# Kernel optimization log

Measured on AMD Instinct MI355X. Metric: run time of the kernel, lower is better.

Reference implementation:

```python
import jax, jax.numpy as jnp
import numpy as np

B, T, C = 2, 2048, 1024
H, DK, OUT = 16, 64, 1024


def setup_inputs() -> dict:
    key = jax.random.key(0)
    k1, k2, k3, k4, k5 = jax.random.split(key, 5)
    glorot_qkv = (2.0 / (C + H * DK)) ** 0.5  # glorot_normal stddev for [C,H,DK]
    glorot_o = (2.0 / (H * DK + OUT)) ** 0.5
    return {
        "x": jax.random.normal(k1, (B, T, C), dtype=jnp.float32),
        "query_mat": jax.random.normal(k2, (C, H, DK), dtype=jnp.float32) * glorot_qkv,
        "key_mat": jax.random.normal(k3, (C, H, DK), dtype=jnp.float32) * glorot_qkv,
        "value_mat": jax.random.normal(k4, (C, H, DK), dtype=jnp.float32) * glorot_qkv,
        "linear_m1": jax.random.normal(k5, (H * DK, OUT), dtype=jnp.float32) * glorot_o,
    }


def reference(x, query_mat, key_mat, value_mat, linear_m1):
    # x: [B,T,C]; projections: [C,H,DK]
    q = jnp.einsum('btc,chd->bhtd', x, query_mat)
    k = jnp.einsum('btc,chd->bhtd', x, key_mat)
    v = jnp.einsum('btc,chd->bhtd', x, value_mat)
    d_k = query_mat.shape[-1]
    # NOTE: faithful to source, which MULTIPLIES by sqrt(d_k)
    w = jnp.einsum('bhtd,bhzd->bhtz', q, k) * (d_k ** 0.5)
    t = w.shape[-1]
    causal = jnp.tril(jnp.ones((t, t), dtype=bool))  # [T,T]
    w = jnp.where(causal, w, -jnp.inf)
    w = jax.nn.softmax(w, axis=-1)
    # dropout inactive (training=False)
    o = jnp.einsum('bhtz,bhzd->bhtd', w, v)
    o = o.transpose(0, 2, 1, 3).reshape(o.shape[0], o.shape[2], -1)  # [B,T,H*DK]
    return jnp.einsum('btc,cz->btz', o, linear_m1)
```

## Files before the change

kernel.cpp:

```cpp
#include <hip/hip_runtime.h>


typedef unsigned short u16;
typedef unsigned int u32;
typedef unsigned long long u64;
typedef __attribute__((ext_vector_type(8))) short bf16x8;
typedef __attribute__((ext_vector_type(4))) float f32x4;

__device__ inline u16 f2bf(float f) {
  union { float f; unsigned u; } v; v.f = f;
  unsigned r = v.u + 0x7FFFu + ((v.u >> 16) & 1u);
  return (u16)(r >> 16);
}
__device__ inline float bf2f(u16 h) {
  union { unsigned u; float f; } v; v.u = ((unsigned)h) << 16;
  return v.f;
}
__device__ inline void glds16(const u16* g, u16* s) {
  __builtin_amdgcn_global_load_lds(
      (const __attribute__((address_space(1))) u32*)g,
      (__attribute__((address_space(3))) u32*)s, 16, 0, 0);
}
#define MFMA __builtin_amdgcn_mfma_f32_16x16x32_bf16

__global__ __launch_bounds__(256) void prep(
    const float* __restrict__ x,
    const float* __restrict__ wq, const float* __restrict__ wk,
    const float* __restrict__ wv, const float* __restrict__ wo,
    u16* __restrict__ Xh, u16* __restrict__ Xl,
    u16* __restrict__ Wqh, u16* __restrict__ Wql,
    u16* __restrict__ Wkh, u16* __restrict__ Wkl,
    u16* __restrict__ Wvt, u16* __restrict__ Wot) {
  const int z = blockIdx.z;
  const int tid = threadIdx.x;
  if (z == 0) {
    const int bid = blockIdx.y * 32 + blockIdx.x;
#pragma unroll
    for (int k = 0; k < 4; k++) {
      int i = bid * 4096 + k * 1024 + tid * 4;
      float4 v = *(const float4*)(x + i);
      ushort4 h, l;
      h.x = f2bf(v.x); l.x = f2bf(v.x - bf2f(h.x));
      h.y = f2bf(v.y); l.y = f2bf(v.y - bf2f(h.y));
      h.z = f2bf(v.z); l.z = f2bf(v.z - bf2f(h.z));
      h.w = f2bf(v.w); l.w = f2bf(v.w - bf2f(h.w));
      *(ushort4*)(Xh + i) = h;
      *(ushort4*)(Xl + i) = l;
    }
    return;
  }
  __shared__ float tile[32][33];
  const float* W = (z == 1) ? wq : (z == 2) ? wk : (z == 3) ? wv : wo;
  const int bx = blockIdx.x * 32, by = blockIdx.y * 32;
  const int tx = tid & 31, ty = tid >> 5;
#pragma unroll
  for (int j = 0; j < 32; j += 8)
    tile[ty + j][tx] = W[(size_t)(by + ty + j) * 1024 + bx + tx];
  __syncthreads();
  if (z <= 2) {
    u16* Th = (z == 1) ? Wqh : Wkh;
    u16* Tl = (z == 1) ? Wql : Wkl;
#pragma unroll
    for (int j = 0; j < 32; j += 8) {
      float v = tile[tx][ty + j];
      u16 h = f2bf(v);
      size_t idx = (size_t)(bx + ty + j) * 1024 + by + tx;
      Th[idx] = h;
      Tl[idx] = f2bf(v - bf2f(h));
    }
  } else {
    u16* T = (z == 3) ? Wvt : Wot;
#pragma unroll
    for (int j = 0; j < 32; j += 8)
      T[(size_t)(bx + ty + j) * 1024 + by + tx] = f2bf(tile[tx][ty + j]);
  }
}

__global__ __launch_bounds__(256) void gemm_qkv(
    const u16* __restrict__ Xh, const u16* __restrict__ Xl,
    const u16* __restrict__ Wqh, const u16* __restrict__ Wql,
    const u16* __restrict__ Wkh, const u16* __restrict__ Wkl,
    const u16* __restrict__ Wvt,
    u16* __restrict__ Qh, u16* __restrict__ Ql,
    u16* __restrict__ Kh, u16* __restrict__ Kl,
    u16* __restrict__ Vt) {
  __shared__ u16 S[4][128][32];
  const int K = 1024;
  const int z = blockIdx.z;
  const bool split = (z < 2);
  const u16* Bh = (z == 0) ? Wqh : (z == 1) ? Wkh : Wvt;
  const u16* Bl = (z == 0) ? Wql : Wkl;
  const int tid = threadIdx.x;
  const int lane = tid & 63, wv = tid >> 6;
  const int quad = lane >> 4, lc = lane & 15;
  const int m0 = blockIdx.y * 128, n0 = blockIdx.x * 128;
  const int wm = (wv >> 1) * 64, wn = (wv & 1) * 64;
  const int lrow = lane >> 2, lk = (lane & 3) * 8;
  const u16* a0p = Xh + (size_t)(m0 + wv * 32 + lrow) * K + lk;
  const u16* a1p = a0p + 16 * K;
  const u16* al0p = Xl + (size_t)(m0 + wv * 32 + lrow) * K + lk;
  const u16* al1p = al0p + 16 * K;
  const u16* b0p = Bh + (size_t)(n0 + wv * 32 + lrow) * K + lk;
  const u16* b1p = b0p + 16 * K;
  const u16* bl0p = split ? (Bl + (size_t)(n0 + wv * 32 + lrow) * K + lk) : b0p;
  const u16* bl1p = bl0p + 16 * K;
  u16* sA0 = &S[0][wv * 32][0];      u16* sA1 = &S[0][wv * 32 + 16][0];
  u16* sAl0 = &S[1][wv * 32][0];     u16* sAl1 = &S[1][wv * 32 + 16][0];
  u16* sB0 = &S[2][wv * 32][0];      u16* sB1 = &S[2][wv * 32 + 16][0];
  u16* sBl0 = &S[3][wv * 32][0];     u16* sBl1 = &S[3][wv * 32 + 16][0];
  f32x4 acc[4][4];
#pragma unroll
  for (int i = 0; i < 4; i++)
#pragma unroll
    for (int j = 0; j < 4; j++) acc[i][j] = (f32x4){0.f, 0.f, 0.f, 0.f};
  for (int kc = 0; kc < K; kc += 32) {
    __syncthreads();
    glds16(a0p + kc, sA0); glds16(a1p + kc, sA1);
    glds16(b0p + kc, sB0); glds16(b1p + kc, sB1);
    if (split) {
      glds16(al0p + kc, sAl0); glds16(al1p + kc, sAl1);
      glds16(bl0p + kc, sBl0); glds16(bl1p + kc, sBl1);
    }
    __syncthreads();
    bf16x8 ah[4], al[4];
#pragma unroll
    for (int mt = 0; mt < 4; mt++)
      ah[mt] = *(const bf16x8*)&S[0][wm + mt * 16 + lc][quad * 8];
    if (split) {
#pragma unroll
      for (int mt = 0; mt < 4; mt++)
        al[mt] = *(const bf16x8*)&S[1][wm + mt * 16 + lc][quad * 8];
    }
#pragma unroll
    for (int nt = 0; nt < 4; nt++) {
      bf16x8 bfh = *(const bf16x8*)&S[2][wn + nt * 16 + lc][quad * 8];
#pragma unroll
      for (int mt = 0; mt < 4; mt++)
        acc[mt][nt] = MFMA(ah[mt], bfh, acc[mt][nt], 0, 0, 0);
      if (split) {
        bf16x8 bfl = *(const bf16x8*)&S[3][wn + nt * 16 + lc][quad * 8];
#pragma unroll
        for (int mt = 0; mt < 4; mt++) {
          acc[mt][nt] = MFMA(ah[mt], bfl, acc[mt][nt], 0, 0, 0);
          acc[mt][nt] = MFMA(al[mt], bfh, acc[mt][nt], 0, 0, 0);
        }
      }
    }
  }
  const int rb = quad * 4;
  if (z == 2) {
#pragma unroll
    for (int mt = 0; mt < 4; mt++)
#pragma unroll
      for (int nt = 0; nt < 4; nt++)
#pragma unroll
        for (int r = 0; r < 4; r++) {
          int m = m0 + wm + mt * 16 + rb + r, n = n0 + wn + nt * 16 + lc;
          int b = m >> 11, t = m & 2047, h = n >> 6, d = n & 63;
          Vt[((size_t)(b * 16 + h) * 64 + d) * 2048 + t] = f2bf(acc[mt][nt][r]);
        }
  } else {
    u16* Ch = (z == 0) ? Qh : Kh;
    u16* Cl = (z == 0) ? Ql : Kl;
    const float scale = (z == 0) ? 8.0f : 1.0f;
#pragma unroll
    for (int mt = 0; mt < 4; mt++)
#pragma unroll
      for (int nt = 0; nt < 4; nt++)
#pragma unroll
        for (int r = 0; r < 4; r++) {
          int m = m0 + wm + mt * 16 + rb + r, n = n0 + wn + nt * 16 + lc;
          int b = m >> 11, t = m & 2047, h = n >> 6, d = n & 63;
          float v = acc[mt][nt][r] * scale;
          u16 hv = f2bf(v);
          size_t idx = ((size_t)(b * 16 + h) * 2048 + t) * 64 + d;
          Ch[idx] = hv;
          Cl[idx] = f2bf(v - bf2f(hv));
        }
  }
}

__global__ __launch_bounds__(256) void gemm_out(const u16* __restrict__ A,
                                                const u16* __restrict__ Bt,
                                                float* __restrict__ C) {
  __shared__ u16 Sa[64][32], Sb[128][32];
  const int K = 1024, N = 1024;
  const int tid = threadIdx.x;
  const int lane = tid & 63, wv = tid >> 6;
  const int quad = lane >> 4, lc = lane & 15;
  const int m0 = blockIdx.y * 64, n0 = blockIdx.x * 128;
  const int wm = (wv >> 1) * 32, wn = (wv & 1) * 64;
  const int lrow = lane >> 2, lk = (lane & 3) * 8;
  const u16* ap = A + (size_t)(m0 + wv * 16 + lrow) * K + lk;
  const u16* b0p = Bt + (size_t)(n0 + wv * 32 + lrow) * K + lk;
  const u16* b1p = b0p + 16 * K;
  u16* sA = &Sa[wv * 16][0];
  u16* sB0 = &Sb[wv * 32][0];
  u16* sB1 = &Sb[wv * 32 + 16][0];
  f32x4 acc[2][4];
#pragma unroll
  for (int i = 0; i < 2; i++)
#pragma unroll
    for (int j = 0; j < 4; j++) acc[i][j] = (f32x4){0.f, 0.f, 0.f, 0.f};
  for (int kc = 0; kc < K; kc += 32) {
    __syncthreads();
    glds16(ap + kc, sA);
    glds16(b0p + kc, sB0);
    glds16(b1p + kc, sB1);
    __syncthreads();
    bf16x8 ah[2];
#pragma unroll
    for (int mt = 0; mt < 2; mt++)
      ah[mt] = *(const bf16x8*)&Sa[wm + mt * 16 + lc][quad * 8];
#pragma unroll
    for (int nt = 0; nt < 4; nt++) {
      bf16x8 bfh = *(const bf16x8*)&Sb[wn + nt * 16 + lc][quad * 8];
#pragma unroll
      for (int mt = 0; mt < 2; mt++)
        acc[mt][nt] = MFMA(ah[mt], bfh, acc[mt][nt], 0, 0, 0);
    }
  }
#pragma unroll
  for (int mt = 0; mt < 2; mt++)
#pragma unroll
    for (int nt = 0; nt < 4; nt++)
#pragma unroll
      for (int r = 0; r < 4; r++)
        C[(size_t)(m0 + wm + mt * 16 + quad * 4 + r) * N + n0 + wn + nt * 16 + lc] =
            acc[mt][nt][r];
}

__global__ __launch_bounds__(256, 2) void attn(const u16* __restrict__ Qh,
                                               const u16* __restrict__ Ql,
                                               const u16* __restrict__ Kh,
                                               const u16* __restrict__ Kl,
                                               const u16* __restrict__ Vt,
                                               u16* __restrict__ O16) {
  __shared__ u16 Khs[2][64][64], Kls[2][64][64], Vs[2][64][64];
  __shared__ u16 Ps[4][16][72];
  const int tid = threadIdx.x;
  const int lane = tid & 63, w = tid >> 6;
  const int quad = lane >> 4, lc = lane & 15;
  const int i = blockIdx.x;
  const int bh = i & 31;
  const int qb = 31 - (i >> 5);
  const int ng = qb + 1;
  const int tq = qb * 64 + w * 16 + lc;
  const size_t kbase = (size_t)bh * 2048 * 64;
  const size_t vbase = (size_t)bh * 64 * 2048;
  const size_t qoff = kbase + (size_t)tq * 64 + quad * 8;
  bf16x8 qh0 = *(const bf16x8*)(Qh + qoff);
  bf16x8 qh1 = *(const bf16x8*)(Qh + qoff + 32);
  bf16x8 ql0 = *(const bf16x8*)(Ql + qoff);
  bf16x8 ql1 = *(const bf16x8*)(Ql + qoff + 32);
  const int srow = lane >> 3;
  const int scol = (lane & 7) ^ srow;
  const u16* kg0 = Kh + kbase + (size_t)(w * 16 + srow) * 64 + scol * 8;
  const u16* lg0 = Kl + kbase + (size_t)(w * 16 + srow) * 64 + scol * 8;
  const u16* vg0 = Vt + vbase + (size_t)(w * 16 + srow) * 2048 + scol * 8;

  float mi = -3.0e38f, li = 0.f;
  f32x4 o[4];
#pragma unroll
  for (int d = 0; d < 4; d++) o[d] = (f32x4){0.f, 0.f, 0.f, 0.f};
  const int rx = lc & 7;

  {
    glds16(kg0, &Khs[0][w * 16][0]); glds16(kg0 + 8 * 64, &Khs[0][w * 16 + 8][0]);
    glds16(lg0, &Kls[0][w * 16][0]); glds16(lg0 + 8 * 64, &Kls[0][w * 16 + 8][0]);
    glds16(vg0, &Vs[0][w * 16][0]);  glds16(vg0 + 8 * 2048, &Vs[0][w * 16 + 8][0]);
  }
  for (int g = 0; g < ng; g++) {
    const int buf = g & 1;
    const int z0 = g * 64;
    __syncthreads();
    if (g + 1 < ng) {
      const int zn = (g + 1) * 64;
      const int nb = buf ^ 1;
      glds16(kg0 + (size_t)zn * 64, &Khs[nb][w * 16][0]);
      glds16(kg0 + (size_t)zn * 64 + 8 * 64, &Khs[nb][w * 16 + 8][0]);
      glds16(lg0 + (size_t)zn * 64, &Kls[nb][w * 16][0]);
      glds16(lg0 + (size_t)zn * 64 + 8 * 64, &Kls[nb][w * 16 + 8][0]);
      glds16(vg0 + zn, &Vs[nb][w * 16][0]);
      glds16(vg0 + zn + 8 * 2048, &Vs[nb][w * 16 + 8][0]);
    }
    f32x4 s[4];
#pragma unroll
    for (int tt = 0; tt < 4; tt++) {
      const int R = tt * 16 + lc;
      bf16x8 kh0 = *(const bf16x8*)&Khs[buf][R][(quad ^ rx) * 8];
      bf16x8 kh1 = *(const bf16x8*)&Khs[buf][R][((4 + quad) ^ rx) * 8];
      bf16x8 kl0 = *(const bf16x8*)&Kls[buf][R][(quad ^ rx) * 8];
      bf16x8 kl1 = *(const bf16x8*)&Kls[buf][R][((4 + quad) ^ rx) * 8];
      f32x4 sv = (f32x4){0.f, 0.f, 0.f, 0.f};
      sv = MFMA(kh0, qh0, sv, 0, 0, 0);
      sv = MFMA(kh1, qh1, sv, 0, 0, 0);
      sv = MFMA(kh0, ql0, sv, 0, 0, 0);
      sv = MFMA(kh1, ql1, sv, 0, 0, 0);
      sv = MFMA(kl0, qh0, sv, 0, 0, 0);
      sv = MFMA(kl1, qh1, sv, 0, 0, 0);
      s[tt] = sv;
    }
    if (g == ng - 1) {
#pragma unroll
      for (int tt = 0; tt < 4; tt++)
#pragma unroll
        for (int r = 0; r < 4; r++)
          if (z0 + tt * 16 + quad * 4 + r > tq) s[tt][r] = -3.0e38f;
    }
    float smax = -3.0e38f;
#pragma unroll
    for (int tt = 0; tt < 4; tt++)
#pragma unroll
      for (int r = 0; r < 4; r++) smax = fmaxf(smax, s[tt][r]);
    smax = fmaxf(smax, __shfl_xor(smax, 16));
    smax = fmaxf(smax, __shfl_xor(smax, 32));
    float mnew = fmaxf(mi, smax);
    float alpha = __expf(mi - mnew);
    mi = mnew;
    float rs = 0.f;
#pragma unroll
    for (int tt = 0; tt < 4; tt++) {
      union { u16 h[4]; u64 d; } pk;
#pragma unroll
      for (int r = 0; r < 4; r++) {
        float p = __expf(s[tt][r] - mnew);
        rs += p;
        pk.h[r] = f2bf(p);
      }
      *(u64*)&Ps[w][lc][tt * 16 + quad * 4] = pk.d;
    }
    li = li * alpha + rs;
#pragma unroll
    for (int d = 0; d < 4; d++) o[d] *= alpha;
    bf16x8 pf0 = *(const bf16x8*)&Ps[w][lc][quad * 8];
    bf16x8 pf1 = *(const bf16x8*)&Ps[w][lc][32 + quad * 8];
#pragma unroll
    for (int dd = 0; dd < 4; dd++) {
      const int R = dd * 16 + lc;
      bf16x8 va0 = *(const bf16x8*)&Vs[buf][R][(quad ^ rx) * 8];
      bf16x8 va1 = *(const bf16x8*)&Vs[buf][R][((4 + quad) ^ rx) * 8];
      o[dd] = MFMA(va0, pf0, o[dd], 0, 0, 0);
      o[dd] = MFMA(va1, pf1, o[dd], 0, 0, 0);
    }
  }
  li += __shfl_xor(li, 16);
  li += __shfl_xor(li, 32);
  const float rli = 1.0f / li;
  const int b = bh >> 4, hh = bh & 15;
  const size_t obase = ((size_t)(b * 2048 + tq)) * 1024 + hh * 64 + quad * 4;
#pragma unroll
  for (int dd = 0; dd < 4; dd++) {
    ushort4 ov;
    ov.x = f2bf(o[dd][0] * rli);
    ov.y = f2bf(o[dd][1] * rli);
    ov.z = f2bf(o[dd][2] * rli);
    ov.w = f2bf(o[dd][3] * rli);
    *(ushort4*)&O16[obase + dd * 16] = ov;
  }
}

extern "C" void kernel_launch(void* const* d_in, const int* in_sizes, int n_in,
                              void* d_out, int out_size, void* d_ws, size_t ws_size,
                              hipStream_t stream) {
  const float* x  = (const float*)d_in[0];
  const float* wq = (const float*)d_in[1];
  const float* wk = (const float*)d_in[2];
  const float* wv = (const float*)d_in[3];
  const float* wo = (const float*)d_in[4];

  char* w = (char*)d_ws;
  const size_t MB = 1u << 20;
  u16* Xh  = (u16*)(w + 0 * MB);
  u16* Xl  = (u16*)(w + 8 * MB);
  u16* Wqh = (u16*)(w + 16 * MB);
  u16* Wql = (u16*)(w + 18 * MB);
  u16* Wkh = (u16*)(w + 20 * MB);
  u16* Wkl = (u16*)(w + 22 * MB);
  u16* Wvt = (u16*)(w + 24 * MB);
  u16* Wot = (u16*)(w + 26 * MB);
  u16* Qhb = (u16*)(w + 28 * MB);
  u16* Qlb = (u16*)(w + 36 * MB);
  u16* Khb = (u16*)(w + 44 * MB);
  u16* Klb = (u16*)(w + 52 * MB);
  u16* Vtb = (u16*)(w + 60 * MB);
  u16* O16 = (u16*)(w + 0 * MB);

  hipLaunchKernelGGL(prep, dim3(32, 32, 5), dim3(256), 0, stream,
                     x, wq, wk, wv, wo, Xh, Xl, Wqh, Wql, Wkh, Wkl, Wvt, Wot);

  hipLaunchKernelGGL(gemm_qkv, dim3(8, 32, 3), dim3(256), 0, stream,
                     Xh, Xl, Wqh, Wql, Wkh, Wkl, Wvt, Qhb, Qlb, Khb, Klb, Vtb);

  hipLaunchKernelGGL(attn, dim3(1024), dim3(256), 0, stream,
                     Qhb, Qlb, Khb, Klb, Vtb, O16);

  hipLaunchKernelGGL(gemm_out, dim3(8, 64), dim3(256), 0, stream, O16, Wot, (float*)d_out);
}
```

Before: 215.0 us.

## Replace QKV and output GEMMs with double-buffered 256x128 pipelined gemm kernel

Both projection GEMMs now run through one templated kernel with 512 threads, 256x128 tiles, K-chunks of 64 and double-buffered LDS filled by async global-to-LDS loads. An XOR swizzle avoids LDS bank conflicts, and explicit vmcnt waits plus barriers and s_setprio interleave loads with MFMA work. The split-precision hi/lo terms are handled as extra K tiles (48 tiles instead of 16), so the three-product sum is kept. This aims to hide global memory latency and raise MFMA utilisation. The hand-scheduled barrier and waitcnt sequence is fragile and could race if counts are wrong, and the larger LDS footprint limits occupancy.

```diff
diff --git a/kernel.cpp b/kernel.cpp
--- a/kernel.cpp
+++ b/kernel.cpp
@@ -76,78 +76,103 @@
   }
 }
 
-__global__ __launch_bounds__(256) void gemm_qkv(
-    const u16* __restrict__ Xh, const u16* __restrict__ Xl,
-    const u16* __restrict__ Wqh, const u16* __restrict__ Wql,
-    const u16* __restrict__ Wkh, const u16* __restrict__ Wkl,
-    const u16* __restrict__ Wvt,
+#define BAR() do { asm volatile("" ::: "memory"); __builtin_amdgcn_s_barrier(); asm volatile("" ::: "memory"); } while (0)
+#define WAITV(N) asm volatile("s_waitcnt vmcnt(" #N ")" ::: "memory")
+#define SP(P) __builtin_amdgcn_s_setprio(P)
+
+template <int MODE>
+__global__ __launch_bounds__(512, 2) void gemm3(
+    const u16* __restrict__ Ah_, const u16* __restrict__ Al_,
+    const u16* __restrict__ BQh, const u16* __restrict__ BQl,
+    const u16* __restrict__ BKh, const u16* __restrict__ BKl,
+    const u16* __restrict__ BVt,
     u16* __restrict__ Qh, u16* __restrict__ Ql,
     u16* __restrict__ Kh, u16* __restrict__ Kl,
-    u16* __restrict__ Vt) {
-  __shared__ u16 S[4][128][32];
-  const int K = 1024;
-  const int z = blockIdx.z;
-  const bool split = (z < 2);
-  const u16* Bh = (z == 0) ? Wqh : (z == 1) ? Wkh : Wvt;
-  const u16* Bl = (z == 0) ? Wql : Wkl;
+    u16* __restrict__ Vt, float* __restrict__ Cout) {
+  __shared__ __align__(16) u16 As[2][256][64];
+  __shared__ __align__(16) u16 Bs[2][128][64];
+  const int z = (MODE == 0) ? blockIdx.z : 3;
+  const u16* Bh_ = (MODE == 1) ? BQh : (z == 0) ? BQh : (z == 1) ? BKh : BVt;
+  const u16* Bl_ = (z == 0) ? BQl : (z == 1) ? BKl : Bh_;
+  const int NT = (MODE == 0 && z < 2) ? 48 : 16;
   const int tid = threadIdx.x;
-  const int lane = tid & 63, wv = tid >> 6;
-  const int quad = lane >> 4, lc = lane & 15;
-  const int m0 = blockIdx.y * 128, n0 = blockIdx.x * 128;
-  const int wm = (wv >> 1) * 64, wn = (wv & 1) * 64;
-  const int lrow = lane >> 2, lk = (lane & 3) * 8;
-  const u16* a0p = Xh + (size_t)(m0 + wv * 32 + lrow) * K + lk;
-  const u16* a1p = a0p + 16 * K;
-  const u16* al0p = Xl + (size_t)(m0 + wv * 32 + lrow) * K + lk;
-  const u16* al1p = al0p + 16 * K;
-  const u16* b0p = Bh + (size_t)(n0 + wv * 32 + lrow) * K + lk;
-  const u16* b1p = b0p + 16 * K;
-  const u16* bl0p = split ? (Bl + (size_t)(n0 + wv * 32 + lrow) * K + lk) : b0p;
-  const u16* bl1p = bl0p + 16 * K;
-  u16* sA0 = &S[0][wv * 32][0];      u16* sA1 = &S[0][wv * 32 + 16][0];
-  u16* sAl0 = &S[1][wv * 32][0];     u16* sAl1 = &S[1][wv * 32 + 16][0];
-  u16* sB0 = &S[2][wv * 32][0];      u16* sB1 = &S[2][wv * 32 + 16][0];
-  u16* sBl0 = &S[3][wv * 32][0];     u16* sBl1 = &S[3][wv * 32 + 16][0];
+  const int lane = tid & 63, wid = tid >> 6;
+  const int quad = lane >> 4, lc = lane & 15, l7 = lane & 7;
+  const int m0 = blockIdx.y * 256, n0 = blockIdx.x * 128;
+  const int wm = (wid >> 1) * 64, wn = (wid & 1) * 64;
+  const int srow = lane >> 3;
+  const int schunk = (lane & 7) ^ (srow & 7);
+  const int ar0 = (wid >> 1) * 64 + (wid & 1) * 16;
+  const int br0 = wid * 16;
+  const size_t aG = (size_t)(m0 + ar0 + srow) * 1024 + schunk * 8;
+  const size_t bG = (size_t)(n0 + br0 + srow) * 1024 + schunk * 8;
+
+#define AREG(T) (((T) < 32) ? Ah_ : Al_)
+#define BREG(T) ((((T) >> 4) == 1) ? Bl_ : Bh_)
+#define COL(T) ((size_t)((T) & 15) * 64)
+#define ST_A0(T, BUF) do { const u16* g_ = AREG(T) + aG + COL(T); \
+    glds16(g_, &As[BUF][ar0][0]); glds16(g_ + 8 * 1024, &As[BUF][ar0 + 8][0]); } while (0)
+#define ST_A1(T, BUF) do { const u16* g_ = AREG(T) + aG + COL(T) + 32 * 1024; \
+    glds16(g_, &As[BUF][ar0 + 32][0]); glds16(g_ + 8 * 1024, &As[BUF][ar0 + 40][0]); } while (0)
+#define ST_B(T, BUF) do { const u16* g_ = BREG(T) + bG + COL(T); \
+    glds16(g_, &Bs[BUF][br0][0]); glds16(g_ + 8 * 1024, &Bs[BUF][br0 + 8][0]); } while (0)
+#define LD_A(BUF, MH) do { _Pragma("unroll") for (int m2 = 0; m2 < 2; m2++) \
+    { _Pragma("unroll") for (int kk = 0; kk < 2; kk++) \
+      afr[m2][kk] = *(const bf16x8*)&As[BUF][wm + (MH) * 32 + m2 * 16 + lc][((kk * 4 + quad) ^ l7) * 8]; } } while (0)
+#define LD_B(BUF) do { _Pragma("unroll") for (int n = 0; n < 4; n++) \
+    { _Pragma("unroll") for (int kk = 0; kk < 2; kk++) \
+      bfr[n][kk] = *(const bf16x8*)&Bs[BUF][wn + n * 16 + lc][((kk * 4 + quad) ^ l7) * 8]; } } while (0)
+#define MM(MH) do { _Pragma("unroll") for (int m2 = 0; m2 < 2; m2++) \
+    { _Pragma("unroll") for (int n = 0; n < 4; n++) \
+      { _Pragma("unroll") for (int kk = 0; kk < 2; kk++) \
+        acc[(MH) * 2 + m2][n] = MFMA(afr[m2][kk], bfr[n][kk], acc[(MH) * 2 + m2][n], 0, 0, 0); } } } while (0)
+
   f32x4 acc[4][4];
 #pragma unroll
-  for (int i = 0; i < 4; i++)
-#pragma unroll
-    for (int j = 0; j < 4; j++) acc[i][j] = (f32x4){0.f, 0.f, 0.f, 0.f};
-  for (int kc = 0; kc < K; kc += 32) {
-    __syncthreads();
-    glds16(a0p + kc, sA0); glds16(a1p + kc, sA1);
-    glds16(b0p + kc, sB0); glds16(b1p + kc, sB1);
-    if (split) {
-      glds16(al0p + kc, sAl0); glds16(al1p + kc, sAl1);
-      glds16(bl0p + kc, sBl0); glds16(bl1p + kc, sBl1);
-    }
-    __syncthreads();
-    bf16x8 ah[4], al[4];
+  for (int mi = 0; mi < 4; mi++)
+#pragma unroll
+    for (int ni = 0; ni < 4; ni++) acc[mi][ni] = (f32x4){0.f, 0.f, 0.f, 0.f};
+  bf16x8 afr[2][2], bfr[4][2];
+
+  ST_A0(0, 0); ST_A1(0, 0); ST_B(0, 0);
+  ST_B(1, 1); ST_A0(1, 1);
+  WAITV(4);
+  BAR();
+
+  const int NI = NT >> 1;
+  for (int i = 0; i < NI; ++i) {
+    const int t1 = 2 * i + 1, t2 = 2 * i + 2, t3 = 2 * i + 3;
+    const bool fin = (t2 >= NT);
+    LD_A(0, 0); LD_B(0);
+    ST_A1(t1, 1);
+    BAR(); SP(1); MM(0); SP(0); BAR();
+    LD_A(0, 1);
+    if (!fin) { ST_B(t2, 0); ST_A0(t2, 0); }
+    BAR(); SP(1); MM(1); SP(0);
+    if (fin) { WAITV(0); } else { WAITV(4); }
+    BAR();
+    LD_A(1, 0); LD_B(1);
+    if (!fin) ST_A1(t2, 0);
+    BAR(); SP(1); MM(0); SP(0); BAR();
+    LD_A(1, 1);
+    if (!fin) { ST_B(t3, 1); ST_A0(t3, 1); }
+    BAR(); SP(1); MM(1); SP(0);
+    if (!fin) { WAITV(4); }
+    BAR();
+  }
+
+  const int rb = quad * 4;
+  if (MODE == 1) {
 #pragma unroll
     for (int mt = 0; mt < 4; mt++)
-      ah[mt] = *(const bf16x8*)&S[0][wm + mt * 16 + lc][quad * 8];
-    if (split) {
-#pragma unroll
-      for (int mt = 0; mt < 4; mt++)
-        al[mt] = *(const bf16x8*)&S[1][wm + mt * 16 + lc][quad * 8];
-    }
-#pragma unroll
-    for (int nt = 0; nt < 4; nt++) {
-      bf16x8 bfh = *(const bf16x8*)&S[2][wn + nt * 16 + lc][quad * 8];
-#pragma unroll
-      for (int mt = 0; mt < 4; mt++)
-        acc[mt][nt] = MFMA(ah[mt], bfh, acc[mt][nt], 0, 0, 0);
-      if (split) {
-        bf16x8 bfl = *(const bf16x8*)&S[3][wn + nt * 16 + lc][quad * 8];
-#pragma unroll
-        for (int mt = 0; mt < 4; mt++) {
-          acc[mt][nt] = MFMA(ah[mt], bfl, acc[mt][nt], 0, 0, 0);
-          acc[mt][nt] = MFMA(al[mt], bfh, acc[mt][nt], 0, 0, 0);
-        }
-      }
-    }
-  }
-  const int rb = quad * 4;
+#pragma unroll
+      for (int nt = 0; nt < 4; nt++)
+#pragma unroll
+        for (int r = 0; r < 4; r++)
+          Cout[(size_t)(m0 + wm + mt * 16 + rb + r) * 1024 + n0 + wn + nt * 16 + lc] =
+              acc[mt][nt][r];
+    return;
+  }
   if (z == 2) {
 #pragma unroll
     for (int mt = 0; mt < 4; mt++)
@@ -178,56 +203,15 @@
           Cl[idx] = f2bf(v - bf2f(hv));
         }
   }
-}
-
-__global__ __launch_bounds__(256) void gemm_out(const u16* __restrict__ A,
-                                                const u16* __restrict__ Bt,
-                                                float* __restrict__ C) {
-  __shared__ u16 Sa[64][32], Sb[128][32];
-  const int K = 1024, N = 1024;
-  const int tid = threadIdx.x;
-  const int lane = tid & 63, wv = tid >> 6;
-  const int quad = lane >> 4, lc = lane & 15;
-  const int m0 = blockIdx.y * 64, n0 = blockIdx.x * 128;
-  const int wm = (wv >> 1) * 32, wn = (wv & 1) * 64;
-  const int lrow = lane >> 2, lk = (lane & 3) * 8;
-  const u16* ap = A + (size_t)(m0 + wv * 16 + lrow) * K + lk;
-  const u16* b0p = Bt + (size_t)(n0 + wv * 32 + lrow) * K + lk;
-  const u16* b1p = b0p + 16 * K;
-  u16* sA = &Sa[wv * 16][0];
-  u16* sB0 = &Sb[wv * 32][0];
-  u16* sB1 = &Sb[wv * 32 + 16][0];
-  f32x4 acc[2][4];
-#pragma unroll
-  for (int i = 0; i < 2; i++)
-#pragma unroll
-    for (int j = 0; j < 4; j++) acc[i][j] = (f32x4){0.f, 0.f, 0.f, 0.f};
-  for (int kc = 0; kc < K; kc += 32) {
-    __syncthreads();
-    glds16(ap + kc, sA);
-    glds16(b0p + kc, sB0);
-    glds16(b1p + kc, sB1);
-    __syncthreads();
-    bf16x8 ah[2];
-#pragma unroll
-    for (int mt = 0; mt < 2; mt++)
-      ah[mt] = *(const bf16x8*)&Sa[wm + mt * 16 + lc][quad * 8];
-#pragma unroll
-    for (int nt = 0; nt < 4; nt++) {
-      bf16x8 bfh = *(const bf16x8*)&Sb[wn + nt * 16 + lc][quad * 8];
-#pragma unroll
-      for (int mt = 0; mt < 2; mt++)
-        acc[mt][nt] = MFMA(ah[mt], bfh, acc[mt][nt], 0, 0, 0);
-    }
-  }
-#pragma unroll
-  for (int mt = 0; mt < 2; mt++)
-#pragma unroll
-    for (int nt = 0; nt < 4; nt++)
-#pragma unroll
-      for (int r = 0; r < 4; r++)
-        C[(size_t)(m0 + wm + mt * 16 + quad * 4 + r) * N + n0 + wn + nt * 16 + lc] =
-            acc[mt][nt][r];
+#undef AREG
+#undef BREG
+#undef COL
+#undef ST_A0
+#undef ST_A1
+#undef ST_B
+#undef LD_A
+#undef LD_B
+#undef MM
 }
 
 __global__ __launch_bounds__(256, 2) void attn(const u16* __restrict__ Qh,
@@ -389,11 +373,15 @@
   hipLaunchKernelGGL(prep, dim3(32, 32, 5), dim3(256), 0, stream,
                      x, wq, wk, wv, wo, Xh, Xl, Wqh, Wql, Wkh, Wkl, Wvt, Wot);
 
-  hipLaunchKernelGGL(gemm_qkv, dim3(8, 32, 3), dim3(256), 0, stream,
-                     Xh, Xl, Wqh, Wql, Wkh, Wkl, Wvt, Qhb, Qlb, Khb, Klb, Vtb);
+  hipLaunchKernelGGL(HIP_KERNEL_NAME(gemm3<0>), dim3(8, 16, 3), dim3(512), 0, stream,
+                     Xh, Xl, Wqh, Wql, Wkh, Wkl, Wvt,
+                     Qhb, Qlb, Khb, Klb, Vtb, (float*)nullptr);
 
   hipLaunchKernelGGL(attn, dim3(1024), dim3(256), 0, stream,
                      Qhb, Qlb, Khb, Klb, Vtb, O16);
 
-  hipLaunchKernelGGL(gemm_out, dim3(8, 64), dim3(256), 0, stream, O16, Wot, (float*)d_out);
-}
+  hipLaunchKernelGGL(HIP_KERNEL_NAME(gemm3<1>), dim3(8, 16, 1), dim3(512), 0, stream,
+                     O16, O16, Wot, Wot, Wot, Wot, Wot,
+                     (u16*)nullptr, (u16*)nullptr, (u16*)nullptr, (u16*)nullptr,
+                     (u16*)nullptr, (float*)d_out);
+}
```

After: 229.2 us. +6.6%, slower.

## Load K-low fragments directly to registers, add exp2 softmax with lazy rescale

Applied to the files above, without the earlier changes.

Removes the K-low shared-memory buffer and reads those fragments straight from global memory into registers. The smaller LDS footprint allows raising the occupancy hint to 3 blocks per SM. Q is pre-scaled by 8·log2(e) so the softmax can use the native exp2. The running-max rescale is skipped when the new max exceeds the old by at most 8, which avoids the per-iteration alpha multiplies. s_setprio raises wave priority around the MFMA sections. The trade-offs are uncoalesced global loads of K-low that sit on the critical path, and extra register pressure.

```diff
diff --git a/kernel.cpp b/kernel.cpp
--- a/kernel.cpp
+++ b/kernel.cpp
@@ -22,6 +22,7 @@
       (__attribute__((address_space(3))) u32*)s, 16, 0, 0);
 }
 #define MFMA __builtin_amdgcn_mfma_f32_16x16x32_bf16
+#define SP(P) __builtin_amdgcn_s_setprio(P)
 
 __global__ __launch_bounds__(256) void prep(
     const float* __restrict__ x,
@@ -162,7 +163,7 @@
   } else {
     u16* Ch = (z == 0) ? Qh : Kh;
     u16* Cl = (z == 0) ? Ql : Kl;
-    const float scale = (z == 0) ? 8.0f : 1.0f;
+    const float scale = (z == 0) ? 11.541560327111707f : 1.0f;
 #pragma unroll
     for (int mt = 0; mt < 4; mt++)
 #pragma unroll
@@ -230,13 +231,13 @@
             acc[mt][nt][r];
 }
 
-__global__ __launch_bounds__(256, 2) void attn(const u16* __restrict__ Qh,
+__global__ __launch_bounds__(256, 3) void attn(const u16* __restrict__ Qh,
                                                const u16* __restrict__ Ql,
                                                const u16* __restrict__ Kh,
                                                const u16* __restrict__ Kl,
                                                const u16* __restrict__ Vt,
                                                u16* __restrict__ O16) {
-  __shared__ u16 Khs[2][64][64], Kls[2][64][64], Vs[2][64][64];
+  __shared__ u16 Khs[2][64][64], Vs[2][64][64];
   __shared__ u16 Ps[4][16][72];
   const int tid = threadIdx.x;
   const int lane = tid & 63, w = tid >> 6;
@@ -256,8 +257,8 @@
   const int srow = lane >> 3;
   const int scol = (lane & 7) ^ srow;
   const u16* kg0 = Kh + kbase + (size_t)(w * 16 + srow) * 64 + scol * 8;
-  const u16* lg0 = Kl + kbase + (size_t)(w * 16 + srow) * 64 + scol * 8;
   const u16* vg0 = Vt + vbase + (size_t)(w * 16 + srow) * 2048 + scol * 8;
+  const u16* klp = Kl + kbase + (size_t)lc * 64 + quad * 8;
 
   float mi = -3.0e38f, li = 0.f;
   f32x4 o[4];
@@ -267,7 +268,6 @@
 
   {
     glds16(kg0, &Khs[0][w * 16][0]); glds16(kg0 + 8 * 64, &Khs[0][w * 16 + 8][0]);
-    glds16(lg0, &Kls[0][w * 16][0]); glds16(lg0 + 8 * 64, &Kls[0][w * 16 + 8][0]);
     glds16(vg0, &Vs[0][w * 16][0]);  glds16(vg0 + 8 * 2048, &Vs[0][w * 16 + 8][0]);
   }
   for (int g = 0; g < ng; g++) {
@@ -279,28 +279,33 @@
       const int nb = buf ^ 1;
       glds16(kg0 + (size_t)zn * 64, &Khs[nb][w * 16][0]);
       glds16(kg0 + (size_t)zn * 64 + 8 * 64, &Khs[nb][w * 16 + 8][0]);
-      glds16(lg0 + (size_t)zn * 64, &Kls[nb][w * 16][0]);
-      glds16(lg0 + (size_t)zn * 64 + 8 * 64, &Kls[nb][w * 16 + 8][0]);
       glds16(vg0 + zn, &Vs[nb][w * 16][0]);
       glds16(vg0 + zn + 8 * 2048, &Vs[nb][w * 16 + 8][0]);
     }
+    const u16* kg = klp + (size_t)z0 * 64;
+    bf16x8 klr0[4], klr1[4];
+#pragma unroll
+    for (int tt = 0; tt < 4; tt++) {
+      klr0[tt] = *(const bf16x8*)(kg + tt * 1024);
+      klr1[tt] = *(const bf16x8*)(kg + tt * 1024 + 32);
+    }
     f32x4 s[4];
+    SP(1);
 #pragma unroll
     for (int tt = 0; tt < 4; tt++) {
       const int R = tt * 16 + lc;
       bf16x8 kh0 = *(const bf16x8*)&Khs[buf][R][(quad ^ rx) * 8];
       bf16x8 kh1 = *(const bf16x8*)&Khs[buf][R][((4 + quad) ^ rx) * 8];
-      bf16x8 kl0 = *(const bf16x8*)&Kls[buf][R][(quad ^ rx) * 8];
-      bf16x8 kl1 = *(const bf16x8*)&Kls[buf][R][((4 + quad) ^ rx) * 8];
       f32x4 sv = (f32x4){0.f, 0.f, 0.f, 0.f};
       sv = MFMA(kh0, qh0, sv, 0, 0, 0);
       sv = MFMA(kh1, qh1, sv, 0, 0, 0);
       sv = MFMA(kh0, ql0, sv, 0, 0, 0);
       sv = MFMA(kh1, ql1, sv, 0, 0, 0);
-      sv = MFMA(kl0, qh0, sv, 0, 0, 0);
-      sv = MFMA(kl1, qh1, sv, 0, 0, 0);
+      sv = MFMA(klr0[tt], qh0, sv, 0, 0, 0);
+      sv = MFMA(klr1[tt], qh1, sv, 0, 0, 0);
       s[tt] = sv;
     }
+    SP(0);
     if (g == ng - 1) {
 #pragma unroll
       for (int tt = 0; tt < 4; tt++)
@@ -315,26 +320,30 @@
       for (int r = 0; r < 4; r++) smax = fmaxf(smax, s[tt][r]);
     smax = fmaxf(smax, __shfl_xor(smax, 16));
     smax = fmaxf(smax, __shfl_xor(smax, 32));
-    float mnew = fmaxf(mi, smax);
-    float alpha = __expf(mi - mnew);
-    mi = mnew;
+    if (!__all(smax - mi <= 8.0f)) {
+      float mnew = fmaxf(mi, smax);
+      float alpha = __builtin_amdgcn_exp2f(mi - mnew);
+      mi = mnew;
+      li *= alpha;
+#pragma unroll
+      for (int d = 0; d < 4; d++) o[d] *= alpha;
+    }
     float rs = 0.f;
 #pragma unroll
     for (int tt = 0; tt < 4; tt++) {
       union { u16 h[4]; u64 d; } pk;
 #pragma unroll
       for (int r = 0; r < 4; r++) {
-        float p = __expf(s[tt][r] - mnew);
+        float p = __builtin_amdgcn_exp2f(s[tt][r] - mi);
         rs += p;
         pk.h[r] = f2bf(p);
       }
       *(u64*)&Ps[w][lc][tt * 16 + quad * 4] = pk.d;
     }
-    li = li * alpha + rs;
-#pragma unroll
-    for (int d = 0; d < 4; d++) o[d] *= alpha;
+    li += rs;
     bf16x8 pf0 = *(const bf16x8*)&Ps[w][lc][quad * 8];
     bf16x8 pf1 = *(const bf16x8*)&Ps[w][lc][32 + quad * 8];
+    SP(1);
 #pragma unroll
     for (int dd = 0; dd < 4; dd++) {
       const int R = dd * 16 + lc;
@@ -343,6 +352,7 @@
       o[dd] = MFMA(va0, pf0, o[dd], 0, 0, 0);
       o[dd] = MFMA(va1, pf1, o[dd], 0, 0, 0);
     }
+    SP(0);
   }
   li += __shfl_xor(li, 16);
   li += __shfl_xor(li, 32);
```

After: 244.0 us. 1.13x slower.
